# Kernel tuning notes

Measured on AMD Instinct MI355X. Metric: run time of the kernel, lower is better.

## Reference

```python
import jax, jax.numpy as jnp
import numpy as np

NUM_HEADS = 8
NORM_GROUPS = 32
EPS = 1e-5


def setup_inputs() -> dict:
    key = jax.random.key(0)
    k1, k2, k3 = jax.random.split(key, 3)
    b, c, h, w = 16, 256, 64, 64
    x = jax.random.normal(k1, (b, c, h, w), dtype=jnp.float32)
    gn_w = jnp.ones((c,), dtype=jnp.float32)
    gn_b = jnp.zeros((c,), dtype=jnp.float32)
    # 1x1 convs == channel matmuls; init like torch (kaiming-ish scale)
    w_qkv = jax.random.normal(k2, (3 * c, c), dtype=jnp.float32) / np.sqrt(c)
    w_proj = jax.random.normal(k3, (c, c), dtype=jnp.float32) / np.sqrt(c)
    b_proj = jnp.zeros((c,), dtype=jnp.float32)
    return {"x": x, "gn_w": gn_w, "gn_b": gn_b, "w_qkv": w_qkv,
            "w_proj": w_proj, "b_proj": b_proj}


def reference(x, gn_w, gn_b, w_qkv, w_proj, b_proj):
    b, c, h, w = x.shape
    H = NUM_HEADS
    d = c // H
    n = h * w
    # GroupNorm over (channels_per_group, h, w)
    xg = x.reshape(b, NORM_GROUPS, -1)
    mu = jnp.mean(xg, axis=-1, keepdims=True)
    var = jnp.mean(jnp.square(xg - mu), axis=-1, keepdims=True)
    xn = ((xg - mu) * jax.lax.rsqrt(var + EPS)).reshape(b, c, h, w)
    xn = xn * gn_w[None, :, None, None] + gn_b[None, :, None, None]
    # 1x1 conv -> (b, 3c, h, w); channel layout is (qkv, heads, d)
    qkv = jnp.einsum('oc,bchw->bohw', w_qkv, xn)
    qkv = qkv.reshape(b, 3, H, d, n)
    q, k, v = qkv[:, 0], qkv[:, 1], qkv[:, 2]  # each (b, H, d, n)
    k = jax.nn.softmax(k, axis=-1)
    # linear attention: small (d x d) state per head
    att = jnp.einsum('bhdn,bhen->bhde', k, v)
    out = jnp.einsum('bhde,bhdn->bhen', att, q)  # (b, H, d, n)
    out = out.reshape(b, c, h, w)
    return jnp.einsum('oc,bchw->bohw', w_proj, out) + b_proj[None, :, None, None]
```

## Files before the change

### kernel.cpp

```cpp
#include <hip/hip_runtime.h>
#include <stdint.h>

#define BATCH 16
#define CCH   256
#define NSP   4096
#define QKV_M 768

typedef unsigned short u16;
typedef short  short8 __attribute__((ext_vector_type(8)));
typedef float  f32x4  __attribute__((ext_vector_type(4)));

__device__ __forceinline__ float bf2f(u16 h) {
  union { unsigned int u; float f; } x; x.u = ((unsigned int)h) << 16; return x.f;
}
__device__ __forceinline__ u16 f2bf(float f) {
  union { float f; unsigned int u; } x; x.f = f;
  unsigned int r = 0x7fffu + ((x.u >> 16) & 1u);
  return (u16)((x.u + r) >> 16);
}

#define GLB(p) ((__attribute__((address_space(1))) void*)(p))
#define LDSP(p) ((__attribute__((address_space(3))) void*)(p))

__global__ __launch_bounds__(256) void convw_kernel(const float* __restrict__ wq,
                                                    const float* __restrict__ wp,
                                                    u16* __restrict__ dst) {
  const int i = (blockIdx.x * 256 + threadIdx.x) * 4;
  float4 v = (i < 196608) ? *(const float4*)(wq + i)
                          : *(const float4*)(wp + (i - 196608));
  ushort4 o;
  o.x = f2bf(v.x); o.y = f2bf(v.y); o.z = f2bf(v.z); o.w = f2bf(v.w);
  *(ushort4*)(dst + i) = o;
}

__global__ __launch_bounds__(256) void gn_stats(const float* __restrict__ x,
                                                float2* __restrict__ stats,
                                                float* __restrict__ att4) {
  const int blk = blockIdx.x;
  const int tid = threadIdx.x;
  {
    float* az = att4 + (size_t)blk * 264;
    for (int i = tid; i < 264; i += 256) az[i] = 0.f;
  }
  const float4* xv = (const float4*)(x + (size_t)blk * 32768);
  float s = 0.f, ss = 0.f;
  for (int i = tid; i < 8192; i += 256) {
    float4 u = xv[i];
    s  += u.x + u.y + u.z + u.w;
    ss += u.x * u.x + u.y * u.y + u.z * u.z + u.w * u.w;
  }
#pragma unroll
  for (int off = 32; off > 0; off >>= 1) {
    s  += __shfl_down(s, off);
    ss += __shfl_down(ss, off);
  }
  __shared__ float red[8];
  const int wave = tid >> 6, lane = tid & 63;
  if (lane == 0) { red[wave * 2] = s; red[wave * 2 + 1] = ss; }
  __syncthreads();
  if (tid == 0) {
    const float S  = red[0] + red[2] + red[4] + red[6];
    const float SS = red[1] + red[3] + red[5] + red[7];
    const float mean = S * (1.f / 32768.f);
    const float var  = SS * (1.f / 32768.f) - mean * mean;
    stats[blk] = make_float2(mean, rsqrtf(var + 1e-5f));
  }
}

__global__ __launch_bounds__(256) void gn_apply_t(const float* __restrict__ x,
                                                  const float* __restrict__ gw,
                                                  const float* __restrict__ gb,
                                                  const float2* __restrict__ stats,
                                                  u16* __restrict__ xnT) {
  __shared__ u16 ls[64][72];
  const int b = blockIdx.z, c0 = blockIdx.y * 64, n0 = blockIdx.x * 64;
  const int tid = threadIdx.x;
#pragma unroll
  for (int r = 0; r < 4; ++r) {
    const int cc = (tid >> 4) + r * 16;
    const int nn = (tid & 15) * 4;
    const int c = c0 + cc;
    const float2 st = stats[b * 32 + (c >> 3)];
    const float wv = gw[c] * st.y;
    const float bv = gb[c] - st.x * wv;
    float4 u = *(const float4*)(x + ((size_t)b * CCH + c) * NSP + n0 + nn);
    ushort4 o;
    o.x = f2bf(u.x * wv + bv);
    o.y = f2bf(u.y * wv + bv);
    o.z = f2bf(u.z * wv + bv);
    o.w = f2bf(u.w * wv + bv);
    *(ushort4*)&ls[cc][nn] = o;
  }
  __syncthreads();
#pragma unroll
  for (int p = 0; p < 2; ++p) {
    const int idx = tid + p * 256;
    const int nn = idx >> 3;
    const int cb = (idx & 7) * 8;
    u16 tmp[8];
#pragma unroll
    for (int j = 0; j < 8; ++j) tmp[j] = ls[cb + j][nn];
    *(uint4*)(xnT + ((size_t)b * NSP + n0 + nn) * CCH + c0 + cb) = *(uint4*)tmp;
  }
}

template <int OUTF32>
__global__ __launch_bounds__(256) void gemm_mfma(const u16* __restrict__ A,
                                                 const u16* __restrict__ Bt,
                                                 const float* __restrict__ bias,
                                                 void* __restrict__ Cm, int M) {
  __shared__ __align__(16) u16 smem[17408];
  const int tid = threadIdx.x, wave = tid >> 6, lane = tid & 63;
  const int n0 = blockIdx.x * 128, m0 = blockIdx.y * 128, bz = blockIdx.z;
  const u16* Bb = Bt + (size_t)bz * (size_t)NSP * CCH;

  const int lrow = lane >> 3;
  const int kcl  = ((lane & 7) ^ lrow) * 8;
  const u16* pA[4]; const u16* pB[4];
#pragma unroll
  for (int j = 0; j < 4; ++j) {
    const int row = j * 32 + wave * 8 + lrow;
    pA[j] = A  + (size_t)(m0 + row) * CCH + kcl;
    pB[j] = Bb + (size_t)(n0 + row) * CCH + kcl;
  }
  u16* lA = smem;
  u16* lB = smem + 8192;

  const int wm = wave >> 1, wn = wave & 1;
  f32x4 acc[4][4];
#pragma unroll
  for (int i = 0; i < 4; ++i)
#pragma unroll
    for (int j = 0; j < 4; ++j) acc[i][j] = (f32x4){0.f, 0.f, 0.f, 0.f};

  for (int it = 0; it < 4; ++it) {
#pragma unroll
    for (int j = 0; j < 4; ++j) {
      __builtin_amdgcn_global_load_lds(GLB(pA[j]), LDSP(lA + (j * 256 + wave * 64) * 8), 16, 0, 0);
      __builtin_amdgcn_global_load_lds(GLB(pB[j]), LDSP(lB + (j * 256 + wave * 64) * 8), 16, 0, 0);
      pA[j] += 64; pB[j] += 64;
    }
    __syncthreads();
#pragma unroll
    for (int w = 0; w < 2; ++w) {
      const int kcf = w * 4 + (lane >> 4);
      short8 af[4], bfr[4];
#pragma unroll
      for (int mt = 0; mt < 4; ++mt) {
        const int row = wm * 64 + mt * 16 + (lane & 15);
        af[mt] = *(const short8*)&lA[(row * 8 + (kcf ^ (row & 7))) * 8];
      }
#pragma unroll
      for (int nt = 0; nt < 4; ++nt) {
        const int row = wn * 64 + nt * 16 + (lane & 15);
        bfr[nt] = *(const short8*)&lB[(row * 8 + (kcf ^ (row & 7))) * 8];
      }
#pragma unroll
      for (int mt = 0; mt < 4; ++mt)
#pragma unroll
        for (int nt = 0; nt < 4; ++nt)
          acc[mt][nt] = __builtin_amdgcn_mfma_f32_16x16x32_bf16(af[mt], bfr[nt], acc[mt][nt], 0, 0, 0);
    }
    __syncthreads();
  }

  if (!OUTF32) {
    u16* cl = smem;
#pragma unroll
    for (int mt = 0; mt < 4; ++mt)
#pragma unroll
      for (int nt = 0; nt < 4; ++nt)
#pragma unroll
        for (int r = 0; r < 4; ++r) {
          const int row = wm * 64 + mt * 16 + (lane >> 4) * 4 + r;
          const int col = wn * 64 + nt * 16 + (lane & 15);
          cl[row * 136 + col] = f2bf(acc[mt][nt][r]);
        }
    __syncthreads();
    u16* C = (u16*)Cm + (size_t)bz * M * NSP;
#pragma unroll
    for (int j = 0; j < 8; ++j) {
      const int idx = tid + j * 256;
      const int row = idx >> 4, chunk = idx & 15;
      *(uint4*)(C + (size_t)(m0 + row) * NSP + n0 + chunk * 8) =
          *(const uint4*)&cl[row * 136 + chunk * 8];
    }
  } else {
    float* clf = (float*)smem;
    float* C = (float*)Cm + (size_t)bz * M * NSP;
#pragma unroll
    for (int pass = 0; pass < 2; ++pass) {
      if (wm == pass) {
#pragma unroll
        for (int mt = 0; mt < 4; ++mt)
#pragma unroll
          for (int nt = 0; nt < 4; ++nt)
#pragma unroll
            for (int r = 0; r < 4; ++r) {
              const int rl = mt * 16 + (lane >> 4) * 4 + r;
              const int col = wn * 64 + nt * 16 + (lane & 15);
              clf[rl * 132 + col] = acc[mt][nt][r] + bias[m0 + pass * 64 + rl];
            }
      }
      __syncthreads();
#pragma unroll
      for (int j = 0; j < 8; ++j) {
        const int idx = tid + j * 256;
        const int row = idx >> 5, chunk = idx & 31;
        *(float4*)(C + (size_t)(m0 + pass * 64 + row) * NSP + n0 + chunk * 4) =
            *(const float4*)&clf[row * 132 + chunk * 4];
      }
      __syncthreads();
    }
  }
}

__global__ __launch_bounds__(256, 4) void att2_kernel(const u16* __restrict__ qkv,
                                                      float* __restrict__ att4) {
  const int b = blockIdx.z, h = blockIdx.y;
  const int bh = b * 8 + h;
  const int tid = threadIdx.x, wave = tid >> 6, lane = tid & 63;
  const int n0 = blockIdx.x * 512 + wave * 128;
  const u16* kp = qkv + ((size_t)b * QKV_M + 256 + h * 32) * NSP;
  const u16* vp = qkv + ((size_t)b * QKV_M + 512 + h * 32) * NSP;
  const int r  = lane & 15;
  const int kc = (lane >> 4) * 8;

  f32x4 acc[2][2], accl[2];
#pragma unroll
  for (int i = 0; i < 2; ++i) {
    accl[i] = (f32x4){0.f, 0.f, 0.f, 0.f};
#pragma unroll
    for (int j = 0; j < 2; ++j) acc[i][j] = (f32x4){0.f, 0.f, 0.f, 0.f};
  }
  short8 ones;
#pragma unroll
  for (int j = 0; j < 8; ++j) ones[j] = (short)0x3F80;

  const size_t base0 = (size_t)r * NSP + (size_t)(n0 + kc);
#pragma unroll
  for (int c = 0; c < 4; ++c) {
    const size_t off = base0 + (size_t)c * 32;
    short8 k0 = *(const short8*)(kp + off);
    short8 k1 = *(const short8*)(kp + off + (size_t)16 * NSP);
    short8 v0 = *(const short8*)(vp + off);
    short8 v1 = *(const short8*)(vp + off + (size_t)16 * NSP);
    short8 e0, e1;
#pragma unroll
    for (int j = 0; j < 8; ++j) {
      e0[j] = (short)f2bf(__expf(bf2f((u16)k0[j])));
      e1[j] = (short)f2bf(__expf(bf2f((u16)k1[j])));
    }
    acc[0][0] = __builtin_amdgcn_mfma_f32_16x16x32_bf16(e0, v0, acc[0][0], 0, 0, 0);
    acc[0][1] = __builtin_amdgcn_mfma_f32_16x16x32_bf16(e0, v1, acc[0][1], 0, 0, 0);
    acc[1][0] = __builtin_amdgcn_mfma_f32_16x16x32_bf16(e1, v0, acc[1][0], 0, 0, 0);
    acc[1][1] = __builtin_amdgcn_mfma_f32_16x16x32_bf16(e1, v1, acc[1][1], 0, 0, 0);
    accl[0]   = __builtin_amdgcn_mfma_f32_16x16x32_bf16(e0, ones, accl[0], 0, 0, 0);
    accl[1]   = __builtin_amdgcn_mfma_f32_16x16x32_bf16(e1, ones, accl[1], 0, 0, 0);
  }

  __shared__ float ratt[4][32][34];
  __shared__ float rl[4][32];
  const int rq = lane >> 4;
#pragma unroll
  for (int dt = 0; dt < 2; ++dt) {
#pragma unroll
    for (int et = 0; et < 2; ++et)
#pragma unroll
      for (int j = 0; j < 4; ++j)
        ratt[wave][dt * 16 + rq * 4 + j][et * 16 + r] = acc[dt][et][j];
    if (r == 0)
#pragma unroll
      for (int j = 0; j < 4; ++j) rl[wave][dt * 16 + rq * 4 + j] = accl[dt][j];
  }
  __syncthreads();
  float* ap = att4 + (size_t)bh * 1056;
  for (int i = tid; i < 1024; i += 256) {
    const int d = i >> 5, e = i & 31;
    atomicAdd(&ap[i], ratt[0][d][e] + ratt[1][d][e] + ratt[2][d][e] + ratt[3][d][e]);
  }
  if (tid < 32)
    atomicAdd(&ap[1024 + tid], rl[0][tid] + rl[1][tid] + rl[2][tid] + rl[3][tid]);
}

__global__ __launch_bounds__(256) void attout_kernel(const u16* __restrict__ qkv,
                                                     const float* __restrict__ att4,
                                                     u16* __restrict__ outT) {
  const int b = blockIdx.z, h = blockIdx.y;
  const int bh = b * 8 + h;
  const int n = blockIdx.x * 256 + threadIdx.x;
  const u16* q = qkv + ((size_t)b * QKV_M + h * 32) * NSP;
  const float* ap = att4 + (size_t)bh * 1056;
  __shared__ float as[32][33];
  for (int i = threadIdx.x; i < 1024; i += 256) {
    const int d = i >> 5;
    as[d][i & 31] = ap[i] / ap[1024 + d];
  }
  __syncthreads();
  float qv[32];
#pragma unroll
  for (int d = 0; d < 32; ++d) qv[d] = bf2f(q[(size_t)d * NSP + n]);
  u16 ob[32];
#pragma unroll
  for (int e = 0; e < 32; ++e) {
    float acc = 0.f;
#pragma unroll
    for (int d = 0; d < 32; ++d) acc += as[d][e] * qv[d];
    ob[e] = f2bf(acc);
  }
  u16* orow = outT + ((size_t)b * NSP + n) * CCH + h * 32;
#pragma unroll
  for (int j = 0; j < 4; ++j) ((uint4*)orow)[j] = ((const uint4*)ob)[j];
}

extern "C" void kernel_launch(void* const* d_in, const int* in_sizes, int n_in,
                              void* d_out, int out_size, void* d_ws, size_t ws_size,
                              hipStream_t stream) {
  const float* x      = (const float*)d_in[0];
  const float* gn_w   = (const float*)d_in[1];
  const float* gn_b   = (const float*)d_in[2];
  const float* w_qkv  = (const float*)d_in[3];
  const float* w_proj = (const float*)d_in[4];
  const float* b_proj = (const float*)d_in[5];
  float* out = (float*)d_out;

  char* ws = (char*)d_ws;
  u16*    xnT   = (u16*)ws;
  u16*    qkv   = (u16*)(ws + 33554432ull);
  float*  att4  = (float*)(ws + 134217728ull);
  float2* stats = (float2*)(ws + 134758400ull);
  u16*    wbf   = (u16*)(ws + 134762496ull);
  u16* wq_bf = wbf;
  u16* wp_bf = wbf + 196608;

  convw_kernel<<<256, 256, 0, stream>>>(w_qkv, w_proj, wbf);
  gn_stats<<<512, 256, 0, stream>>>(x, stats, att4);
  gn_apply_t<<<dim3(64, 4, 16), 256, 0, stream>>>(x, gn_w, gn_b, stats, xnT);
  gemm_mfma<0><<<dim3(32, 6, 16), 256, 0, stream>>>(wq_bf, xnT, nullptr, qkv, QKV_M);
  att2_kernel<<<dim3(8, 8, 16), 256, 0, stream>>>(qkv, att4);
  attout_kernel<<<dim3(16, 8, 16), 256, 0, stream>>>(qkv, att4, xnT);
  gemm_mfma<1><<<dim3(32, 2, 16), 256, 0, stream>>>(wp_bf, xnT, b_proj, out, CCH);
}
```

Baseline: 258.6 us.

## Fold attention state into projection weights and write Q transposed from QKV GEMM

Replaces the attention-output kernel with a small per-batch kernel that premultiplies the projection weights by the normalized per-head attention state, giving W2 = Wp·blockdiag(att). The final GEMM then reads Q directly instead of a materialized attention-output tensor. To make Q readable as the B operand, the QKV GEMM writes the Q rows (m0<256) transposed into n-major layout through LDS. This drops a full pass that wrote and reread a bf16 activation tensor, at the cost of a transposed LDS store with possible bank conflicts and an extra bf16 rounding of the combined weights.

```diff
diff --git a/kernel.cpp b/kernel.cpp
--- a/kernel.cpp
+++ b/kernel.cpp
@@ -104,15 +104,17 @@
   }
 }
 
-template <int OUTF32>
+template <int OUTF32, int TRQ>
 __global__ __launch_bounds__(256) void gemm_mfma(const u16* __restrict__ A,
                                                  const u16* __restrict__ Bt,
                                                  const float* __restrict__ bias,
-                                                 void* __restrict__ Cm, int M) {
+                                                 void* __restrict__ Cm, int M,
+                                                 int aBatch, long btStride) {
   __shared__ __align__(16) u16 smem[17408];
   const int tid = threadIdx.x, wave = tid >> 6, lane = tid & 63;
   const int n0 = blockIdx.x * 128, m0 = blockIdx.y * 128, bz = blockIdx.z;
-  const u16* Bb = Bt + (size_t)bz * (size_t)NSP * CCH;
+  const u16* Ab = A + (size_t)bz * aBatch;
+  const u16* Bb = Bt + (size_t)bz * btStride;
 
   const int lrow = lane >> 3;
   const int kcl  = ((lane & 7) ^ lrow) * 8;
@@ -120,7 +122,7 @@
 #pragma unroll
   for (int j = 0; j < 4; ++j) {
     const int row = j * 32 + wave * 8 + lrow;
-    pA[j] = A  + (size_t)(m0 + row) * CCH + kcl;
+    pA[j] = Ab + (size_t)(m0 + row) * CCH + kcl;
     pB[j] = Bb + (size_t)(n0 + row) * CCH + kcl;
   }
   u16* lA = smem;
@@ -166,6 +168,7 @@
 
   if (!OUTF32) {
     u16* cl = smem;
+    const bool tr = TRQ && (m0 < 256);
 #pragma unroll
     for (int mt = 0; mt < 4; ++mt)
 #pragma unroll
@@ -174,16 +177,27 @@
         for (int r = 0; r < 4; ++r) {
           const int row = wm * 64 + mt * 16 + (lane >> 4) * 4 + r;
           const int col = wn * 64 + nt * 16 + (lane & 15);
-          cl[row * 136 + col] = f2bf(acc[mt][nt][r]);
+          if (tr) cl[col * 136 + row] = f2bf(acc[mt][nt][r]);
+          else    cl[row * 136 + col] = f2bf(acc[mt][nt][r]);
         }
     __syncthreads();
     u16* C = (u16*)Cm + (size_t)bz * M * NSP;
-#pragma unroll
-    for (int j = 0; j < 8; ++j) {
-      const int idx = tid + j * 256;
-      const int row = idx >> 4, chunk = idx & 15;
-      *(uint4*)(C + (size_t)(m0 + row) * NSP + n0 + chunk * 8) =
-          *(const uint4*)&cl[row * 136 + chunk * 8];
+    if (tr) {
+#pragma unroll
+      for (int j = 0; j < 8; ++j) {
+        const int idx = tid + j * 256;
+        const int nl = idx >> 4, mc = (idx & 15) * 8;
+        *(uint4*)(C + (size_t)(n0 + nl) * CCH + m0 + mc) =
+            *(const uint4*)&cl[nl * 136 + mc];
+      }
+    } else {
+#pragma unroll
+      for (int j = 0; j < 8; ++j) {
+        const int idx = tid + j * 256;
+        const int row = idx >> 4, chunk = idx & 15;
+        *(uint4*)(C + (size_t)(m0 + row) * NSP + n0 + chunk * 8) =
+            *(const uint4*)&cl[row * 136 + chunk * 8];
+      }
     }
   } else {
     float* clf = (float*)smem;
@@ -283,34 +297,32 @@
     atomicAdd(&ap[1024 + tid], rl[0][tid] + rl[1][tid] + rl[2][tid] + rl[3][tid]);
 }
 
-__global__ __launch_bounds__(256) void attout_kernel(const u16* __restrict__ qkv,
-                                                     const float* __restrict__ att4,
-                                                     u16* __restrict__ outT) {
-  const int b = blockIdx.z, h = blockIdx.y;
-  const int bh = b * 8 + h;
-  const int n = blockIdx.x * 256 + threadIdx.x;
-  const u16* q = qkv + ((size_t)b * QKV_M + h * 32) * NSP;
-  const float* ap = att4 + (size_t)bh * 1056;
-  __shared__ float as[32][33];
-  for (int i = threadIdx.x; i < 1024; i += 256) {
-    const int d = i >> 5;
-    as[d][i & 31] = ap[i] / ap[1024 + d];
-  }
-  __syncthreads();
-  float qv[32];
-#pragma unroll
-  for (int d = 0; d < 32; ++d) qv[d] = bf2f(q[(size_t)d * NSP + n]);
-  u16 ob[32];
-#pragma unroll
-  for (int e = 0; e < 32; ++e) {
+__global__ __launch_bounds__(256) void w2_kernel(const u16* __restrict__ wp_bf,
+                                                 const float* __restrict__ att4,
+                                                 u16* __restrict__ W2) {
+  const int b = blockIdx.x >> 4;
+  const int o0 = (blockIdx.x & 15) * 16;
+  const int tid = threadIdx.x;
+  const int h = tid >> 5, d = tid & 31;
+  const float* ap = att4 + ((size_t)b * 8 + h) * 1056;
+  const float linv = 1.f / ap[1024 + d];
+  float as[32];
+#pragma unroll
+  for (int e = 0; e < 32; ++e) as[e] = ap[d * 32 + e] * linv;
+  u16* w2p = W2 + (size_t)b * 65536;
+  for (int oi = 0; oi < 16; ++oi) {
+    const int o = o0 + oi;
+    const uint4* wr = (const uint4*)(wp_bf + o * 256 + h * 32);
     float acc = 0.f;
 #pragma unroll
-    for (int d = 0; d < 32; ++d) acc += as[d][e] * qv[d];
-    ob[e] = f2bf(acc);
-  }
-  u16* orow = outT + ((size_t)b * NSP + n) * CCH + h * 32;
-#pragma unroll
-  for (int j = 0; j < 4; ++j) ((uint4*)orow)[j] = ((const uint4*)ob)[j];
+    for (int j = 0; j < 4; ++j) {
+      uint4 u = wr[j];
+      const u16* w8 = (const u16*)&u;
+#pragma unroll
+      for (int t = 0; t < 8; ++t) acc += bf2f(w8[t]) * as[j * 8 + t];
+    }
+    w2p[o * 256 + tid] = f2bf(acc);
+  }
 }
 
 extern "C" void kernel_launch(void* const* d_in, const int* in_sizes, int n_in,
@@ -332,12 +344,15 @@
   u16*    wbf   = (u16*)(ws + 134762496ull);
   u16* wq_bf = wbf;
   u16* wp_bf = wbf + 196608;
+  u16* W2 = xnT;
 
   convw_kernel<<<256, 256, 0, stream>>>(w_qkv, w_proj, wbf);
   gn_stats<<<512, 256, 0, stream>>>(x, stats, att4);
   gn_apply_t<<<dim3(64, 4, 16), 256, 0, stream>>>(x, gn_w, gn_b, stats, xnT);
-  gemm_mfma<0><<<dim3(32, 6, 16), 256, 0, stream>>>(wq_bf, xnT, nullptr, qkv, QKV_M);
+  gemm_mfma<0, 1><<<dim3(32, 6, 16), 256, 0, stream>>>(wq_bf, xnT, nullptr, qkv,
+                                                       QKV_M, 0, (long)NSP * CCH);
   att2_kernel<<<dim3(8, 8, 16), 256, 0, stream>>>(qkv, att4);
-  attout_kernel<<<dim3(16, 8, 16), 256, 0, stream>>>(qkv, att4, xnT);
-  gemm_mfma<1><<<dim3(32, 2, 16), 256, 0, stream>>>(wp_bf, xnT, b_proj, out, CCH);
-}
+  w2_kernel<<<256, 256, 0, stream>>>(wp_bf, att4, W2);
+  gemm_mfma<1, 0><<<dim3(32, 2, 16), 256, 0, stream>>>(W2, qkv, b_proj, out,
+                                                       CCH, 65536, (long)QKV_M * NSP);
+}
```

New measurement: 234.3 us. 9.4% less time.
